# Kernel optimization log

Measured on AMD Instinct MI355X. Metric: run time of the kernel, lower is better.

Reference implementation:

```python
import jax, jax.numpy as jnp
import numpy as np

B, S, D = 32, 4096, 512  # batch, src seq len, hidden (n_hidden_in == n_hidden_out)


def setup_inputs() -> dict:
    key = jax.random.key(0)
    k1, k2, k3, k4 = jax.random.split(key, 4)
    return {
        "hidden_targ": jax.random.normal(k1, (B, D), dtype=jnp.float32),
        "hidden_src": jax.random.normal(k2, (B, S, D), dtype=jnp.float32),
        "mask": jnp.ones((B, S), dtype=jnp.float32),
        "W": jax.random.normal(k3, (D, 2 * D), dtype=jnp.float32) * (2 * D) ** -0.5,
        "V": jax.random.uniform(k4, (D,), dtype=jnp.float32),
    }


def reference(hidden_targ, hidden_src, mask, W, V):
    # W @ cat(targ, src) == targ @ Wt^T + src @ Ws^T  (avoids materializing the
    # repeated/concatenated [b, s, 2d] tensor the torch code builds)
    d = hidden_targ.shape[-1]
    Wt, Ws = W[:, :d], W[:, d:]
    # [b, 1, h] + [b, s, h] -> tanh pre-activation
    pre = jnp.tanh(
        jnp.einsum("bd,hd->bh", hidden_targ, Wt)[:, None, :]
        + jnp.einsum("bsd,hd->bsh", hidden_src, Ws)
    )
    e = jnp.einsum("bsh,h->bs", pre, V)            # scores [b, s]
    att_weights = jax.nn.softmax(e, axis=1) * mask  # softmax then mask (as in source)
    ctx = jnp.einsum("bs,bsd->bd", att_weights, hidden_src)
    hidden_output = ctx + hidden_targ
    return att_weights, hidden_output
```

## Files before the change

### kernel.cpp

```cpp
#include <hip/hip_runtime.h>
#include <hip/hip_bf16.h>


typedef __attribute__((ext_vector_type(8))) short bf16x8;
typedef __attribute__((ext_vector_type(4))) float f32x4;

#define BM 128
#define BKK 32
#define LDA 40

static __device__ __forceinline__ unsigned cvt2(float a, float b) {
    union { __hip_bfloat162 h; unsigned u; } v;
    v.h = __float22bfloat162_rn(make_float2(a, b));
    return v.u;
}

static __device__ __forceinline__ void async_load16(const void* g, void* l) {
    __builtin_amdgcn_global_load_lds(
        (const __attribute__((address_space(1))) void*)g,
        (__attribute__((address_space(3))) void*)l, 16, 0, 0);
}

static __device__ __forceinline__ float fast_tanh(float x) {
    float ex = exp2f(x * 2.8853900817779268f);
    return 1.0f - 2.0f / (ex + 1.0f);
}

#define WS_WBF     0L
#define WS_EPART   524288L
#define WS_E       2621440L
#define WS_T       3145728L
#define WS_STATS   3211264L
#define WS_CTXP    3211520L

__global__ void wconv_kernel(const float* __restrict__ W, short* __restrict__ wbf) {
    const int gid = blockIdx.x * 256 + threadIdx.x;
    const int tile = gid >> 9, p = gid & 511;
    const int hx = tile >> 4, ktile = tile & 15;
    const int r = p >> 2, up = p & 3;
    const int u = up ^ ((r >> 1) & 3);
    const float* s = W + (long)(hx * 128 + r) * 1024 + 512 + ktile * 32 + u * 8;
    float4 v0 = *(const float4*)(s);
    float4 v1 = *(const float4*)(s + 4);
    uint4 pk;
    pk.x = cvt2(v0.x, v0.y); pk.y = cvt2(v0.z, v0.w);
    pk.z = cvt2(v1.x, v1.y); pk.w = cvt2(v1.z, v1.w);
    ((uint4*)wbf)[gid] = pk;
}

__global__ void t_kernel(const float* __restrict__ targ,
                         const float* __restrict__ W,
                         float* __restrict__ t) {
    __shared__ float tg[512];
    const int b = blockIdx.x >> 2;
    const int hbase = (blockIdx.x & 3) * 128;
    const int tid = threadIdx.x;
    tg[tid]       = targ[b * 512 + tid];
    tg[tid + 256] = targ[b * 512 + tid + 256];
    __syncthreads();
    const int lane = tid & 63, wave = tid >> 6;
    for (int h = hbase + wave; h < hbase + 128; h += 4) {
        const float* wr = W + (long)h * 1024;
        float s = 0.f;
        #pragma unroll
        for (int i = 0; i < 2; i++) {
            const int d = lane * 4 + i * 256;
            float4 wv = *(const float4*)(wr + d);
            s += wv.x * tg[d] + wv.y * tg[d + 1] + wv.z * tg[d + 2] + wv.w * tg[d + 3];
        }
        s += __shfl_xor(s, 1);  s += __shfl_xor(s, 2);  s += __shfl_xor(s, 4);
        s += __shfl_xor(s, 8);  s += __shfl_xor(s, 16); s += __shfl_xor(s, 32);
        if (lane == 0) t[b * 512 + h] = s;
    }
}

__global__ __launch_bounds__(256, 2)
void gemm_kernel(const float* __restrict__ src,
                 const short* __restrict__ wbf,
                 const float* __restrict__ t,
                 const float* __restrict__ V,
                 float* __restrict__ epart) {
    __shared__ __align__(16) short As[BM * LDA];
    __shared__ __align__(16) short Bs[4096];
    __shared__ float er[2][128];

    const int tid = threadIdx.x;
    const int L = blockIdx.x;
    const int mt = (L >> 5) * 8 + (L & 7);
    const int hx = (L >> 3) & 3;
    const long m0 = (long)mt * BM;
    const int b = (int)(m0 >> 12);

    const int lane = tid & 63;
    const int wave = tid >> 6;
    const int wm = wave & 1, wn = wave >> 1;
    const int lr = lane & 15, quad = lane >> 4;

    f32x4 acc[4][4];
    #pragma unroll
    for (int i = 0; i < 4; i++)
        #pragma unroll
        for (int j = 0; j < 4; j++)
            acc[i][j] = (f32x4){0.f, 0.f, 0.f, 0.f};

    const int arow = tid >> 1, ah = (tid & 1) * 16;

    for (int kt = 0; kt < 512; kt += BKK) {
        __syncthreads();
        const short* chunk = wbf + (long)(hx * 16 + (kt >> 5)) * 4096;
        async_load16(chunk + tid * 8, Bs + tid * 8);
        async_load16(chunk + 2048 + tid * 8, Bs + 2048 + tid * 8);
        const float* ap = src + (m0 + arow) * 512 + kt + ah;
        float4 v0 = *(const float4*)(ap);
        float4 v1 = *(const float4*)(ap + 4);
        float4 v2 = *(const float4*)(ap + 8);
        float4 v3 = *(const float4*)(ap + 12);
        uint4 pA, pB;
        pA.x = cvt2(v0.x, v0.y); pA.y = cvt2(v0.z, v0.w);
        pA.z = cvt2(v1.x, v1.y); pA.w = cvt2(v1.z, v1.w);
        pB.x = cvt2(v2.x, v2.y); pB.y = cvt2(v2.z, v2.w);
        pB.z = cvt2(v3.x, v3.y); pB.w = cvt2(v3.z, v3.w);
        *(uint4*)(As + arow * LDA + ah)     = pA;
        *(uint4*)(As + arow * LDA + ah + 8) = pB;
        __syncthreads();

        bf16x8 af[4], bfr[4];
        #pragma unroll
        for (int mi = 0; mi < 4; mi++)
            af[mi] = *(const bf16x8*)(As + (wm * 64 + mi * 16 + lr) * LDA + quad * 8);
        #pragma unroll
        for (int ni = 0; ni < 4; ni++) {
            const int row = wn * 64 + ni * 16 + lr;
            const int q = quad ^ ((row >> 1) & 3);
            bfr[ni] = *(const bf16x8*)(Bs + row * 32 + q * 8);
        }
        #pragma unroll
        for (int mi = 0; mi < 4; mi++)
            #pragma unroll
            for (int ni = 0; ni < 4; ni++)
                acc[mi][ni] = __builtin_amdgcn_mfma_f32_16x16x32_bf16(
                    af[mi], bfr[ni], acc[mi][ni], 0, 0, 0);
    }

    const float* trow = t + b * 512;
    float th[4], vv[4];
    #pragma unroll
    for (int ni = 0; ni < 4; ni++) {
        const int h = hx * 128 + wn * 64 + ni * 16 + lr;
        th[ni] = trow[h];
        vv[ni] = V[h];
    }
    #pragma unroll
    for (int mi = 0; mi < 4; mi++) {
        #pragma unroll
        for (int r = 0; r < 4; r++) {
            float es = 0.f;
            #pragma unroll
            for (int ni = 0; ni < 4; ni++)
                es += fast_tanh(acc[mi][ni][r] + th[ni]) * vv[ni];
            es += __shfl_xor(es, 1);
            es += __shfl_xor(es, 2);
            es += __shfl_xor(es, 4);
            es += __shfl_xor(es, 8);
            if (lr == 0) er[wn][wm * 64 + mi * 16 + quad * 4 + r] = es;
        }
    }
    __syncthreads();
    if (tid < 128)
        epart[(long)hx * 131072 + m0 + tid] = er[0][tid] + er[1][tid];
}

__global__ void stats_kernel(const float* __restrict__ epart,
                             float* __restrict__ e, float* __restrict__ stats) {
    const int b = blockIdx.x, tid = threadIdx.x;
    __shared__ float red[256];
    float ev[16];
    float mx = -1e30f;
    #pragma unroll
    for (int i = 0; i < 16; i++) {
        const long m = (long)b * 4096 + tid + i * 256;
        float v = epart[m] + epart[131072 + m] + epart[262144 + m] + epart[393216 + m];
        e[m] = v;
        ev[i] = v;
        mx = fmaxf(mx, v);
    }
    red[tid] = mx; __syncthreads();
    for (int st = 128; st > 0; st >>= 1) {
        if (tid < st) red[tid] = fmaxf(red[tid], red[tid + st]);
        __syncthreads();
    }
    mx = red[0]; __syncthreads();
    float sm = 0.f;
    #pragma unroll
    for (int i = 0; i < 16; i++)
        sm += exp2f((ev[i] - mx) * 1.4426950408889634f);
    red[tid] = sm; __syncthreads();
    for (int st = 128; st > 0; st >>= 1) {
        if (tid < st) red[tid] += red[tid + st];
        __syncthreads();
    }
    if (tid == 0) { stats[b * 2] = mx; stats[b * 2 + 1] = red[0]; }
}

__global__ __launch_bounds__(256)
void ctx_kernel(const float* __restrict__ e, const float* __restrict__ stats,
                const float* __restrict__ mask, const float* __restrict__ src,
                float* __restrict__ att, float* __restrict__ ctxpart) {
    const int b = blockIdx.y;
    const int s0 = blockIdx.x * 256;
    const int tid = threadIdx.x;
    __shared__ float ash[256];
    __shared__ float4 part[128];

    const float mx = stats[b * 2];
    const float inv = 1.0f / stats[b * 2 + 1];
    const int s = s0 + tid;
    float a = exp2f((e[b * 4096 + s] - mx) * 1.4426950408889634f) * inv
              * mask[b * 4096 + s];
    att[(long)b * 4096 + s] = a;
    ash[tid] = a;
    __syncthreads();

    const int half = tid >> 7, d4 = tid & 127;
    float4 acc = {0.f, 0.f, 0.f, 0.f};
    const float4* s4 = (const float4*)(src + ((long)b * 4096 + s0) * 512);
    #pragma unroll 4
    for (int i = half; i < 256; i += 2) {
        float4 v = s4[(long)i * 128 + d4];
        float w = ash[i];
        acc.x += w * v.x; acc.y += w * v.y; acc.z += w * v.z; acc.w += w * v.w;
    }
    if (half) part[d4] = acc;
    __syncthreads();
    if (!half) {
        float4 p = part[d4];
        acc.x += p.x; acc.y += p.y; acc.z += p.z; acc.w += p.w;
        *(float4*)(ctxpart + ((long)blockIdx.x * 32 + b) * 512 + d4 * 4) = acc;
    }
}

__global__ void final_kernel(const float* __restrict__ targ,
                             const float* __restrict__ ctxpart,
                             float* __restrict__ outh) {
    const int g = blockIdx.x * 256 + threadIdx.x;
    float sv = targ[g];
    #pragma unroll
    for (int x = 0; x < 16; x++) sv += ctxpart[(long)x * 16384 + g];
    outh[g] = sv;
}

extern "C" void kernel_launch(void* const* d_in, const int* in_sizes, int n_in,
                              void* d_out, int out_size, void* d_ws, size_t ws_size,
                              hipStream_t stream) {
    const float* targ = (const float*)d_in[0];
    const float* src  = (const float*)d_in[1];
    const float* mask = (const float*)d_in[2];
    const float* W    = (const float*)d_in[3];
    const float* V    = (const float*)d_in[4];

    float* att  = (float*)d_out;
    float* outh = (float*)d_out + 131072;

    char* ws = (char*)d_ws;
    short* wbf    = (short*)(ws + WS_WBF);
    float* epart  = (float*)(ws + WS_EPART);
    float* e      = (float*)(ws + WS_E);
    float* t      = (float*)(ws + WS_T);
    float* st     = (float*)(ws + WS_STATS);
    float* ctxp   = (float*)(ws + WS_CTXP);

    wconv_kernel<<<128, 256, 0, stream>>>(W, wbf);
    t_kernel<<<128, 256, 0, stream>>>(targ, W, t);
    gemm_kernel<<<4096, 256, 0, stream>>>(src, wbf, t, V, epart);
    stats_kernel<<<32, 256, 0, stream>>>(epart, e, st);
    ctx_kernel<<<dim3(16, 32), 256, 0, stream>>>(e, st, mask, src, att, ctxp);
    final_kernel<<<64, 256, 0, stream>>>(targ, ctxp, outh);
}
```

Before: 494.5 us.

## Fuse GEMM, local softmax and context reduction into one kernel using an SMEM-resident src tile

Each block now holds a 128-row bf16 tile of src in shared memory (128 KB, swizzled) and loops over all four h-blocks, so src is read from global memory once instead of four times for the GEMM plus once more for the context. A block-local max and sum give a flash-style partial softmax, and the context partial is computed from the shared bf16 tile. A small final kernel merges the per-tile stats and partials. Two kernel launches and the epart round trip go away. In exchange, occupancy drops to one block per CU, and the context is now accumulated from bf16 values rather than fp32, which lowers its precision.

```diff
diff --git a/kernel.cpp b/kernel.cpp
--- a/kernel.cpp
+++ b/kernel.cpp
@@ -5,33 +5,31 @@
 typedef __attribute__((ext_vector_type(8))) short bf16x8;
 typedef __attribute__((ext_vector_type(4))) float f32x4;
 
-#define BM 128
-#define BKK 32
-#define LDA 40
+#define L2E 1.4426950408889634f
 
 static __device__ __forceinline__ unsigned cvt2(float a, float b) {
     union { __hip_bfloat162 h; unsigned u; } v;
     v.h = __float22bfloat162_rn(make_float2(a, b));
     return v.u;
 }
-
+static __device__ __forceinline__ float bits2f(unsigned u) {
+    union { unsigned u; float f; } x; x.u = u; return x.f;
+}
 static __device__ __forceinline__ void async_load16(const void* g, void* l) {
     __builtin_amdgcn_global_load_lds(
         (const __attribute__((address_space(1))) void*)g,
         (__attribute__((address_space(3))) void*)l, 16, 0, 0);
 }
-
 static __device__ __forceinline__ float fast_tanh(float x) {
     float ex = exp2f(x * 2.8853900817779268f);
     return 1.0f - 2.0f / (ex + 1.0f);
 }
 
-#define WS_WBF     0L
-#define WS_EPART   524288L
-#define WS_E       2621440L
-#define WS_T       3145728L
-#define WS_STATS   3211264L
-#define WS_CTXP    3211520L
+#define WS_WBF   0L
+#define WS_T     524288L
+#define WS_E     589824L
+#define WS_MST   1114112L
+#define WS_CTXP  1122304L
 
 __global__ void wconv_kernel(const float* __restrict__ W, short* __restrict__ wbf) {
     const int gid = blockIdx.x * 256 + threadIdx.x;
@@ -74,179 +72,198 @@
     }
 }
 
-__global__ __launch_bounds__(256, 2)
-void gemm_kernel(const float* __restrict__ src,
-                 const short* __restrict__ wbf,
-                 const float* __restrict__ t,
-                 const float* __restrict__ V,
-                 float* __restrict__ epart) {
-    __shared__ __align__(16) short As[BM * LDA];
-    __shared__ __align__(16) short Bs[4096];
+__global__ __launch_bounds__(256, 1)
+void fused_kernel(const float* __restrict__ src,
+                  const short* __restrict__ wbf,
+                  const float* __restrict__ t,
+                  const float* __restrict__ V,
+                  const float* __restrict__ mask,
+                  float* __restrict__ e_ws,
+                  float* __restrict__ mstats,
+                  float* __restrict__ ctxp) {
+    __shared__ __align__(16) short As[128 * 512];
+    __shared__ __align__(16) short Bs[2][4096];
     __shared__ float er[2][128];
+    __shared__ float pbuf[128];
+    __shared__ float red[8];
 
     const int tid = threadIdx.x;
-    const int L = blockIdx.x;
-    const int mt = (L >> 5) * 8 + (L & 7);
-    const int hx = (L >> 3) & 3;
-    const long m0 = (long)mt * BM;
-    const int b = (int)(m0 >> 12);
-
-    const int lane = tid & 63;
-    const int wave = tid >> 6;
+    const int mt  = blockIdx.x;
+    const int b   = mt >> 5;
+    const long m0 = (long)mt * 128;
+
+    const int lane = tid & 63, wave = tid >> 6;
     const int wm = wave & 1, wn = wave >> 1;
     const int lr = lane & 15, quad = lane >> 4;
-
-    f32x4 acc[4][4];
-    #pragma unroll
-    for (int i = 0; i < 4; i++)
-        #pragma unroll
-        for (int j = 0; j < 4; j++)
-            acc[i][j] = (f32x4){0.f, 0.f, 0.f, 0.f};
-
+    const int l7 = lr & 7;
     const int arow = tid >> 1, ah = (tid & 1) * 16;
 
-    for (int kt = 0; kt < 512; kt += BKK) {
-        __syncthreads();
-        const short* chunk = wbf + (long)(hx * 16 + (kt >> 5)) * 4096;
-        async_load16(chunk + tid * 8, Bs + tid * 8);
-        async_load16(chunk + 2048 + tid * 8, Bs + 2048 + tid * 8);
-        const float* ap = src + (m0 + arow) * 512 + kt + ah;
-        float4 v0 = *(const float4*)(ap);
-        float4 v1 = *(const float4*)(ap + 4);
-        float4 v2 = *(const float4*)(ap + 8);
-        float4 v3 = *(const float4*)(ap + 12);
-        uint4 pA, pB;
-        pA.x = cvt2(v0.x, v0.y); pA.y = cvt2(v0.z, v0.w);
-        pA.z = cvt2(v1.x, v1.y); pA.w = cvt2(v1.z, v1.w);
-        pB.x = cvt2(v2.x, v2.y); pB.y = cvt2(v2.z, v2.w);
-        pB.z = cvt2(v3.x, v3.y); pB.w = cvt2(v3.z, v3.w);
-        *(uint4*)(As + arow * LDA + ah)     = pA;
-        *(uint4*)(As + arow * LDA + ah + 8) = pB;
-        __syncthreads();
-
-        bf16x8 af[4], bfr[4];
-        #pragma unroll
-        for (int mi = 0; mi < 4; mi++)
-            af[mi] = *(const bf16x8*)(As + (wm * 64 + mi * 16 + lr) * LDA + quad * 8);
+    async_load16(wbf + tid * 8, &Bs[0][0] + tid * 8);
+    async_load16(wbf + 2048 + tid * 8, &Bs[0][0] + 2048 + tid * 8);
+
+    for (int hx = 0; hx < 4; ++hx) {
+        f32x4 acc[4][4];
+        #pragma unroll
+        for (int i = 0; i < 4; i++)
+            #pragma unroll
+            for (int j = 0; j < 4; j++)
+                acc[i][j] = (f32x4){0.f, 0.f, 0.f, 0.f};
+
+        for (int kt = 0; kt < 16; ++kt) {
+            const int idx = hx * 16 + kt;
+            __syncthreads();
+            if (idx < 63) {
+                const short* cn = wbf + (long)(idx + 1) * 4096;
+                short* bd = &Bs[(idx + 1) & 1][0];
+                async_load16(cn + tid * 8, bd + tid * 8);
+                async_load16(cn + 2048 + tid * 8, bd + 2048 + tid * 8);
+            }
+            if (hx == 0) {
+                const float* ap = src + (m0 + arow) * 512 + kt * 32 + ah;
+                float4 v0 = *(const float4*)(ap);
+                float4 v1 = *(const float4*)(ap + 4);
+                float4 v2 = *(const float4*)(ap + 8);
+                float4 v3 = *(const float4*)(ap + 12);
+                uint4 pA, pB;
+                pA.x = cvt2(v0.x, v0.y); pA.y = cvt2(v0.z, v0.w);
+                pA.z = cvt2(v1.x, v1.y); pA.w = cvt2(v1.z, v1.w);
+                pB.x = cvt2(v2.x, v2.y); pB.y = cvt2(v2.z, v2.w);
+                pB.z = cvt2(v3.x, v3.y); pB.w = cvt2(v3.z, v3.w);
+                const int c0 = kt * 4 + (tid & 1) * 2;
+                const int r7 = arow & 7;
+                *(uint4*)(As + arow * 512 + ((c0    ) ^ r7) * 8) = pA;
+                *(uint4*)(As + arow * 512 + ((c0 + 1) ^ r7) * 8) = pB;
+                __syncthreads();
+            }
+
+            bf16x8 af[4], bfr[4];
+            const short* bsrc = &Bs[idx & 1][0];
+            #pragma unroll
+            for (int mi = 0; mi < 4; mi++) {
+                const int row = wm * 64 + mi * 16 + lr;
+                af[mi] = *(const bf16x8*)(As + row * 512 + (((kt * 4 + quad) ^ l7) * 8));
+            }
+            #pragma unroll
+            for (int ni = 0; ni < 4; ni++) {
+                const int row = wn * 64 + ni * 16 + lr;
+                const int q = quad ^ ((row >> 1) & 3);
+                bfr[ni] = *(const bf16x8*)(bsrc + row * 32 + q * 8);
+            }
+            #pragma unroll
+            for (int mi = 0; mi < 4; mi++)
+                #pragma unroll
+                for (int ni = 0; ni < 4; ni++)
+                    acc[mi][ni] = __builtin_amdgcn_mfma_f32_16x16x32_bf16(
+                        af[mi], bfr[ni], acc[mi][ni], 0, 0, 0);
+        }
+
+        const float* trow = t + b * 512;
+        float th[4], vv[4];
         #pragma unroll
         for (int ni = 0; ni < 4; ni++) {
-            const int row = wn * 64 + ni * 16 + lr;
-            const int q = quad ^ ((row >> 1) & 3);
-            bfr[ni] = *(const bf16x8*)(Bs + row * 32 + q * 8);
-        }
-        #pragma unroll
-        for (int mi = 0; mi < 4; mi++)
-            #pragma unroll
-            for (int ni = 0; ni < 4; ni++)
-                acc[mi][ni] = __builtin_amdgcn_mfma_f32_16x16x32_bf16(
-                    af[mi], bfr[ni], acc[mi][ni], 0, 0, 0);
-    }
-
-    const float* trow = t + b * 512;
-    float th[4], vv[4];
-    #pragma unroll
-    for (int ni = 0; ni < 4; ni++) {
-        const int h = hx * 128 + wn * 64 + ni * 16 + lr;
-        th[ni] = trow[h];
-        vv[ni] = V[h];
-    }
-    #pragma unroll
-    for (int mi = 0; mi < 4; mi++) {
-        #pragma unroll
-        for (int r = 0; r < 4; r++) {
-            float es = 0.f;
-            #pragma unroll
-            for (int ni = 0; ni < 4; ni++)
-                es += fast_tanh(acc[mi][ni][r] + th[ni]) * vv[ni];
-            es += __shfl_xor(es, 1);
-            es += __shfl_xor(es, 2);
-            es += __shfl_xor(es, 4);
-            es += __shfl_xor(es, 8);
-            if (lr == 0) er[wn][wm * 64 + mi * 16 + quad * 4 + r] = es;
-        }
-    }
-    __syncthreads();
-    if (tid < 128)
-        epart[(long)hx * 131072 + m0 + tid] = er[0][tid] + er[1][tid];
-}
-
-__global__ void stats_kernel(const float* __restrict__ epart,
-                             float* __restrict__ e, float* __restrict__ stats) {
+            const int h = hx * 128 + wn * 64 + ni * 16 + lr;
+            th[ni] = trow[h];
+            vv[ni] = V[h];
+        }
+        #pragma unroll
+        for (int mi = 0; mi < 4; mi++) {
+            #pragma unroll
+            for (int r = 0; r < 4; r++) {
+                float es = 0.f;
+                #pragma unroll
+                for (int ni = 0; ni < 4; ni++)
+                    es += fast_tanh(acc[mi][ni][r] + th[ni]) * vv[ni];
+                es += __shfl_xor(es, 1);
+                es += __shfl_xor(es, 2);
+                es += __shfl_xor(es, 4);
+                es += __shfl_xor(es, 8);
+                if (lr == 0) {
+                    float* slot = &er[wn][wm * 64 + mi * 16 + quad * 4 + r];
+                    if (hx == 0) *slot = es; else *slot += es;
+                }
+            }
+        }
+    }
+
+    __syncthreads();
+    const bool valid = tid < 128;
+    float myE = valid ? (er[0][tid] + er[1][tid]) : -1e30f;
+    float mx = myE;
+    #pragma unroll
+    for (int m = 1; m <= 32; m <<= 1) mx = fmaxf(mx, __shfl_xor(mx, m));
+    if (lane == 0) red[wave] = mx;
+    __syncthreads();
+    const float mL = fmaxf(fmaxf(red[0], red[1]), fmaxf(red[2], red[3]));
+    float pv = valid ? exp2f((myE - mL) * L2E) : 0.f;
+    float sv = pv;
+    #pragma unroll
+    for (int m = 1; m <= 32; m <<= 1) sv += __shfl_xor(sv, m);
+    if (lane == 0) red[4 + wave] = sv;
+    if (valid) {
+        e_ws[m0 + tid] = myE;
+        pbuf[tid] = pv * mask[m0 + tid];
+    }
+    if (tid == 0) mstats[mt * 2] = mL;
+    __syncthreads();
+    if (tid == 0) mstats[mt * 2 + 1] = red[4] + red[5] + red[6] + red[7];
+
+    const int d0 = tid * 2;
+    const int cb = d0 >> 3;
+    const int coff = d0 & 7;
+    float a0 = 0.f, a1 = 0.f;
+    #pragma unroll 4
+    for (int s = 0; s < 128; ++s) {
+        const unsigned u = *(const unsigned*)(As + s * 512 + ((cb ^ (s & 7)) * 8) + coff);
+        const float w = pbuf[s];
+        a0 += w * bits2f(u << 16);
+        a1 += w * bits2f(u & 0xffff0000u);
+    }
+    ctxp[(long)mt * 512 + d0]     = a0;
+    ctxp[(long)mt * 512 + d0 + 1] = a1;
+}
+
+__global__ void final2_kernel(const float* __restrict__ e_ws,
+                              const float* __restrict__ mstats,
+                              const float* __restrict__ ctxp,
+                              const float* __restrict__ mask,
+                              const float* __restrict__ targ,
+                              float* __restrict__ att,
+                              float* __restrict__ outh) {
     const int b = blockIdx.x, tid = threadIdx.x;
-    __shared__ float red[256];
-    float ev[16];
-    float mx = -1e30f;
+    __shared__ float wL[32];
+    __shared__ float bc[2];
+    if (tid < 64) {
+        const int lane = tid;
+        float mv = -1e30f, sv = 0.f;
+        if (lane < 32) {
+            mv = mstats[(b * 32 + lane) * 2];
+            sv = mstats[(b * 32 + lane) * 2 + 1];
+        }
+        float M = mv;
+        #pragma unroll
+        for (int m = 1; m <= 32; m <<= 1) M = fmaxf(M, __shfl_xor(M, m));
+        float sc = sv * exp2f((mv - M) * L2E);
+        #pragma unroll
+        for (int m = 1; m <= 32; m <<= 1) sc += __shfl_xor(sc, m);
+        if (lane < 32) wL[lane] = exp2f((mv - M) * L2E) / sc;
+        if (lane == 0) { bc[0] = M; bc[1] = sc; }
+    }
+    __syncthreads();
+    const float M = bc[0], invS = 1.0f / bc[1];
     #pragma unroll
     for (int i = 0; i < 16; i++) {
-        const long m = (long)b * 4096 + tid + i * 256;
-        float v = epart[m] + epart[131072 + m] + epart[262144 + m] + epart[393216 + m];
-        e[m] = v;
-        ev[i] = v;
-        mx = fmaxf(mx, v);
-    }
-    red[tid] = mx; __syncthreads();
-    for (int st = 128; st > 0; st >>= 1) {
-        if (tid < st) red[tid] = fmaxf(red[tid], red[tid + st]);
-        __syncthreads();
-    }
-    mx = red[0]; __syncthreads();
-    float sm = 0.f;
-    #pragma unroll
-    for (int i = 0; i < 16; i++)
-        sm += exp2f((ev[i] - mx) * 1.4426950408889634f);
-    red[tid] = sm; __syncthreads();
-    for (int st = 128; st > 0; st >>= 1) {
-        if (tid < st) red[tid] += red[tid + st];
-        __syncthreads();
-    }
-    if (tid == 0) { stats[b * 2] = mx; stats[b * 2 + 1] = red[0]; }
-}
-
-__global__ __launch_bounds__(256)
-void ctx_kernel(const float* __restrict__ e, const float* __restrict__ stats,
-                const float* __restrict__ mask, const float* __restrict__ src,
-                float* __restrict__ att, float* __restrict__ ctxpart) {
-    const int b = blockIdx.y;
-    const int s0 = blockIdx.x * 256;
-    const int tid = threadIdx.x;
-    __shared__ float ash[256];
-    __shared__ float4 part[128];
-
-    const float mx = stats[b * 2];
-    const float inv = 1.0f / stats[b * 2 + 1];
-    const int s = s0 + tid;
-    float a = exp2f((e[b * 4096 + s] - mx) * 1.4426950408889634f) * inv
-              * mask[b * 4096 + s];
-    att[(long)b * 4096 + s] = a;
-    ash[tid] = a;
-    __syncthreads();
-
-    const int half = tid >> 7, d4 = tid & 127;
-    float4 acc = {0.f, 0.f, 0.f, 0.f};
-    const float4* s4 = (const float4*)(src + ((long)b * 4096 + s0) * 512);
-    #pragma unroll 4
-    for (int i = half; i < 256; i += 2) {
-        float4 v = s4[(long)i * 128 + d4];
-        float w = ash[i];
-        acc.x += w * v.x; acc.y += w * v.y; acc.z += w * v.z; acc.w += w * v.w;
-    }
-    if (half) part[d4] = acc;
-    __syncthreads();
-    if (!half) {
-        float4 p = part[d4];
-        acc.x += p.x; acc.y += p.y; acc.z += p.z; acc.w += p.w;
-        *(float4*)(ctxpart + ((long)blockIdx.x * 32 + b) * 512 + d4 * 4) = acc;
-    }
-}
-
-__global__ void final_kernel(const float* __restrict__ targ,
-                             const float* __restrict__ ctxpart,
-                             float* __restrict__ outh) {
-    const int g = blockIdx.x * 256 + threadIdx.x;
-    float sv = targ[g];
-    #pragma unroll
-    for (int x = 0; x < 16; x++) sv += ctxpart[(long)x * 16384 + g];
-    outh[g] = sv;
+        const int s = i * 256 + tid;
+        const long idx = (long)b * 4096 + s;
+        att[idx] = exp2f((e_ws[idx] - M) * L2E) * invS * mask[idx];
+    }
+    #pragma unroll
+    for (int dd = 0; dd < 2; dd++) {
+        const int d = dd * 256 + tid;
+        float a = targ[b * 512 + d];
+        for (int L = 0; L < 32; L++)
+            a += wL[L] * ctxp[((long)(b * 32 + L)) * 512 + d];
+        outh[b * 512 + d] = a;
+    }
 }
 
 extern "C" void kernel_launch(void* const* d_in, const int* in_sizes, int n_in,
@@ -262,17 +279,14 @@
     float* outh = (float*)d_out + 131072;
 
     char* ws = (char*)d_ws;
-    short* wbf    = (short*)(ws + WS_WBF);
-    float* epart  = (float*)(ws + WS_EPART);
-    float* e      = (float*)(ws + WS_E);
-    float* t      = (float*)(ws + WS_T);
-    float* st     = (float*)(ws + WS_STATS);
-    float* ctxp   = (float*)(ws + WS_CTXP);
+    short* wbf   = (short*)(ws + WS_WBF);
+    float* t     = (float*)(ws + WS_T);
+    float* e     = (float*)(ws + WS_E);
+    float* mst   = (float*)(ws + WS_MST);
+    float* ctxp  = (float*)(ws + WS_CTXP);
 
     wconv_kernel<<<128, 256, 0, stream>>>(W, wbf);
     t_kernel<<<128, 256, 0, stream>>>(targ, W, t);
-    gemm_kernel<<<4096, 256, 0, stream>>>(src, wbf, t, V, epart);
-    stats_kernel<<<32, 256, 0, stream>>>(epart, e, st);
-    ctx_kernel<<<dim3(16, 32), 256, 0, stream>>>(e, st, mask, src, att, ctxp);
-    final_kernel<<<64, 256, 0, stream>>>(targ, ctxp, outh);
-}
+    fused_kernel<<<1024, 256, 0, stream>>>(src, wbf, t, V, mask, e, mst, ctxp);
+    final2_kernel<<<32, 256, 0, stream>>>(e, mst, ctxp, mask, targ, att, outh);
+}
```

After: 599.4 us. 1.21x slower.
